# Kernel optimization log

Measured on AMD Instinct MI355X. Metric: run time of the kernel, lower is better.

The kernel has to match this reference:

```python
import jax, jax.numpy as jnp
import numpy as np

N_NODES = 50000
N_EDGES = 800000
HIDDEN = 64
NUM_FEATURES = 1
OUT_DIM = 2


def setup_inputs() -> dict:
    key = jax.random.key(0)
    k = jax.random.split(key, 6)
    x = jax.random.normal(k[0], (N_NODES, NUM_FEATURES), dtype=jnp.float32)
    edge_index = jax.random.randint(k[1], (2, N_EDGES), 0, N_NODES, dtype=jnp.int32)
    # GCNConv params (PyG default: glorot weight, zero bias; random here for testing)
    W1 = jax.random.normal(k[2], (NUM_FEATURES, HIDDEN), dtype=jnp.float32) * 0.5
    b1 = jax.random.normal(k[3], (HIDDEN,), dtype=jnp.float32) * 0.1
    W2 = jax.random.normal(k[4], (HIDDEN, OUT_DIM), dtype=jnp.float32) * 0.1
    b2 = jax.random.normal(k[5], (OUT_DIM,), dtype=jnp.float32) * 0.1
    return {"x": x, "edge_index": edge_index, "W1": W1, "b1": b1, "W2": W2, "b2": b2}


def _gcn_norm(edge_index, num_nodes):
    # PyG gcn_norm with add_self_loops=True, symmetric normalization
    row, col = edge_index[0], edge_index[1]
    loop = jnp.arange(num_nodes, dtype=row.dtype)
    row = jnp.concatenate([row, loop])
    col = jnp.concatenate([col, loop])
    ew = jnp.ones(row.shape[0], dtype=jnp.float32)
    deg = jax.ops.segment_sum(ew, col, num_segments=num_nodes)  # in-degree incl. self-loop
    dinv = jnp.where(deg > 0, jax.lax.rsqrt(deg), 0.0)
    norm = dinv[row] * dinv[col]  # [E+N]
    return row, col, norm


def _gcn_conv(x, row, col, norm, W, b, num_nodes):
    h = x @ W                                  # [N, out] transform first (out <= in here is fine)
    msg = h[row] * norm[:, None]               # gather + scale, [E+N, out]
    out = jax.ops.segment_sum(msg, col, num_segments=num_nodes)  # scatter-add at targets
    return out + b


def reference(x, edge_index, W1, b1, W2, b2):
    row, col, norm = _gcn_norm(edge_index, N_NODES)
    h = _gcn_conv(x, row, col, norm, W1, b1, N_NODES)
    h = jax.nn.relu(h)
    out = _gcn_conv(h, row, col, norm, W2, b2, N_NODES)
    return out
```

## Files before the change

### kernel.cpp

```cpp
#include <hip/hip_runtime.h>
#include <math.h>

#define N_NODES 50000
#define N_EDGES 800000
#define HIDDEN  64
#define NPART   500
#define PCHUNK  1600
#define NB      256
#define SL      196
#define CAPB    32
#define BCAP    3600


__global__ __launch_bounds__(256)
void k_part(const int* __restrict__ row, const int* __restrict__ col,
            unsigned* __restrict__ tails, unsigned* __restrict__ bks) {
    __shared__ unsigned stage[NB * CAPB];
    __shared__ unsigned cnt[NB], gpos[NB];
    const int t  = threadIdx.x;
    const int e0 = blockIdx.x * PCHUNK;
    cnt[t] = 0u;
    __syncthreads();
    const int4* c4 = (const int4*)(col + e0);
    const int4* r4 = (const int4*)(row + e0);
    for (int i = t; i < PCHUNK / 4; i += 256) {
        int4 cv = c4[i];
        int4 rv = r4[i];
#pragma unroll
        for (int k = 0; k < 4; ++k) {
            int c = (&cv.x)[k], r = (&rv.x)[k];
            int b = c / SL;
            unsigned off = atomicAdd(&cnt[b], 1u);
            if (off < CAPB)
                stage[(b << 5) + off] = ((unsigned)(c - b * SL) << 16) | (unsigned)r;
        }
    }
    __syncthreads();
    {
        unsigned cc = min(cnt[t], (unsigned)CAPB);
        cnt[t]  = cc;
        gpos[t] = atomicAdd(&tails[t], cc);
    }
    __syncthreads();
    for (int i = t; i < NB * CAPB; i += 256) {
        int b = i >> 5; unsigned o = (unsigned)(i & 31);
        if (o < cnt[b]) {
            unsigned dst = gpos[b] + o;
            if (dst < BCAP) bks[(size_t)b * BCAP + dst] = stage[i];
        }
    }
}

__global__ __launch_bounds__(256)
void k_dg(const unsigned* __restrict__ tails, const unsigned* __restrict__ bks,
          const float* __restrict__ x, float* __restrict__ dinv, float* __restrict__ g) {
    __shared__ unsigned acc[SL];
    const int t = threadIdx.x, b = blockIdx.x;
    if (t < SL) acc[t] = 0u;
    __syncthreads();
    unsigned tail = min(tails[b], (unsigned)BCAP);
    const unsigned* bk = bks + (size_t)b * BCAP;
    const uint4* bk4 = (const uint4*)bk;
    unsigned hv = tail & ~3u;
    for (unsigned i = t; (i << 2) < hv; i += 256) {
        uint4 v = bk4[i];
        atomicAdd(&acc[v.x >> 16], 1u);
        atomicAdd(&acc[v.y >> 16], 1u);
        atomicAdd(&acc[v.z >> 16], 1u);
        atomicAdd(&acc[v.w >> 16], 1u);
    }
    for (unsigned i = hv + t; i < tail; i += 256)
        atomicAdd(&acc[bk[i] >> 16], 1u);
    __syncthreads();
    if (t < SL) {
        int n = b * SL + t;
        if (n < N_NODES) {
            float di = rsqrtf((float)(acc[t] + 1u));
            dinv[n] = di;
            g[n] = di * x[n];
        }
    }
}

__global__ __launch_bounds__(256)
void k_a1(const unsigned* __restrict__ tails, const unsigned* __restrict__ bks,
          const float* __restrict__ g, const float* __restrict__ dinv,
          const float* __restrict__ W1, const float* __restrict__ b1,
          const float* __restrict__ W2, float2* __restrict__ z) {
    __shared__ float acc[SL];
    const int t = threadIdx.x, b = blockIdx.x;
    if (t < SL) acc[t] = 0.0f;
    __syncthreads();
    unsigned tail = min(tails[b], (unsigned)BCAP);
    const unsigned* bk = bks + (size_t)b * BCAP;
    const uint4* bk4 = (const uint4*)bk;
    unsigned hv = tail & ~3u;
    for (unsigned i = t; (i << 2) < hv; i += 256) {
        uint4 v = bk4[i];
        float g0 = g[v.x & 0xFFFFu];
        float g1 = g[v.y & 0xFFFFu];
        float g2 = g[v.z & 0xFFFFu];
        float g3 = g[v.w & 0xFFFFu];
        atomicAdd(&acc[v.x >> 16], g0);
        atomicAdd(&acc[v.y >> 16], g1);
        atomicAdd(&acc[v.z >> 16], g2);
        atomicAdd(&acc[v.w >> 16], g3);
    }
    for (unsigned i = hv + t; i < tail; i += 256) {
        unsigned v = bk[i];
        atomicAdd(&acc[v >> 16], g[v & 0xFFFFu]);
    }
    __syncthreads();
    if (t < SL) {
        int n = b * SL + t;
        if (n < N_NODES) {
            float di = dinv[n];
            float sv = di * (acc[t] + g[n]);
            float y0 = 0.0f, y1 = 0.0f;
#pragma unroll
            for (int k = 0; k < HIDDEN; ++k) {
                float h = fmaxf(sv * W1[k] + b1[k], 0.0f);
                y0 += h * W2[2 * k];
                y1 += h * W2[2 * k + 1];
            }
            z[n] = make_float2(di * y0, di * y1);
        }
    }
}

__global__ __launch_bounds__(256)
void k_a2(const unsigned* __restrict__ tails, const unsigned* __restrict__ bks,
          const float2* __restrict__ z, const float* __restrict__ dinv,
          const float* __restrict__ b2, float2* __restrict__ out) {
    __shared__ float ax[SL];
    __shared__ float ay[SL];
    const int t = threadIdx.x, b = blockIdx.x;
    if (t < SL) { ax[t] = 0.0f; ay[t] = 0.0f; }
    __syncthreads();
    unsigned tail = min(tails[b], (unsigned)BCAP);
    const unsigned* bk = bks + (size_t)b * BCAP;
    const uint4* bk4 = (const uint4*)bk;
    unsigned hv = tail & ~3u;
    for (unsigned i = t; (i << 2) < hv; i += 256) {
        uint4 v = bk4[i];
        float2 z0 = z[v.x & 0xFFFFu];
        float2 z1 = z[v.y & 0xFFFFu];
        float2 z2 = z[v.z & 0xFFFFu];
        float2 z3 = z[v.w & 0xFFFFu];
        atomicAdd(&ax[v.x >> 16], z0.x); atomicAdd(&ay[v.x >> 16], z0.y);
        atomicAdd(&ax[v.y >> 16], z1.x); atomicAdd(&ay[v.y >> 16], z1.y);
        atomicAdd(&ax[v.z >> 16], z2.x); atomicAdd(&ay[v.z >> 16], z2.y);
        atomicAdd(&ax[v.w >> 16], z3.x); atomicAdd(&ay[v.w >> 16], z3.y);
    }
    for (unsigned i = hv + t; i < tail; i += 256) {
        unsigned v = bk[i];
        float2 zz = z[v & 0xFFFFu];
        atomicAdd(&ax[v >> 16], zz.x);
        atomicAdd(&ay[v >> 16], zz.y);
    }
    __syncthreads();
    if (t < SL) {
        int n = b * SL + t;
        if (n < N_NODES) {
            float di = dinv[n];
            float2 zn = z[n];
            out[n] = make_float2(di * (ax[t] + zn.x) + b2[0],
                                 di * (ay[t] + zn.y) + b2[1]);
        }
    }
}


extern "C" void kernel_launch(void* const* d_in, const int* in_sizes, int n_in,
                              void* d_out, int out_size, void* d_ws, size_t ws_size,
                              hipStream_t stream) {
    const float* x  = (const float*)d_in[0];
    const int*   ei = (const int*)d_in[1];
    const float* W1 = (const float*)d_in[2];
    const float* b1 = (const float*)d_in[3];
    const float* W2 = (const float*)d_in[4];
    const float* b2 = (const float*)d_in[5];

    const int* row = ei;
    const int* col = ei + N_EDGES;

    char* p = (char*)d_ws;
    unsigned* tails = (unsigned*)p;  p += 1024 + 128;
    unsigned* bks   = (unsigned*)p;  p += (size_t)NB * BCAP * 4;
    float*    dinv  = (float*)p;     p += 200064;
    float*    g     = (float*)p;     p += 200064;
    float2*   z     = (float2*)p;

    hipMemsetAsync(tails, 0, NB * sizeof(unsigned), stream);
    k_part<<<NPART, 256, 0, stream>>>(row, col, tails, bks);
    k_dg  <<<NB,    256, 0, stream>>>(tails, bks, x, dinv, g);
    k_a1  <<<NB,    256, 0, stream>>>(tails, bks, g, dinv, W1, b1, W2, z);
    k_a2  <<<NB,    256, 0, stream>>>(tails, bks, z, dinv, b2, (float2*)d_out);
}
```

Before: 107.9 us.

## Fold degree counting into partition kernel and drop separate degree pass

Degree counting moves out of its own kernel into the partition kernel, which now does a global atomic increment per edge. The aggregation kernels recompute rsqrt(deg+1) and the x scaling per gathered source instead of reading precomputed dinv and g arrays. This removes one kernel launch and one extra pass over the bucketed edge lists. The cost is 800k global atomics spread over random addresses, plus two gathers and an rsqrt per edge in the first aggregation instead of one gather.

```diff
diff --git a/kernel.cpp b/kernel.cpp
--- a/kernel.cpp
+++ b/kernel.cpp
@@ -14,7 +14,8 @@
 
 __global__ __launch_bounds__(256)
 void k_part(const int* __restrict__ row, const int* __restrict__ col,
-            unsigned* __restrict__ tails, unsigned* __restrict__ bks) {
+            unsigned* __restrict__ tails, unsigned* __restrict__ bks,
+            unsigned* __restrict__ deg) {
     __shared__ unsigned stage[NB * CAPB];
     __shared__ unsigned cnt[NB], gpos[NB];
     const int t  = threadIdx.x;
@@ -29,6 +30,7 @@
 #pragma unroll
         for (int k = 0; k < 4; ++k) {
             int c = (&cv.x)[k], r = (&rv.x)[k];
+            atomicAdd(&deg[c], 1u);
             int b = c / SL;
             unsigned off = atomicAdd(&cnt[b], 1u);
             if (off < CAPB)
@@ -52,39 +54,8 @@
 }
 
 __global__ __launch_bounds__(256)
-void k_dg(const unsigned* __restrict__ tails, const unsigned* __restrict__ bks,
-          const float* __restrict__ x, float* __restrict__ dinv, float* __restrict__ g) {
-    __shared__ unsigned acc[SL];
-    const int t = threadIdx.x, b = blockIdx.x;
-    if (t < SL) acc[t] = 0u;
-    __syncthreads();
-    unsigned tail = min(tails[b], (unsigned)BCAP);
-    const unsigned* bk = bks + (size_t)b * BCAP;
-    const uint4* bk4 = (const uint4*)bk;
-    unsigned hv = tail & ~3u;
-    for (unsigned i = t; (i << 2) < hv; i += 256) {
-        uint4 v = bk4[i];
-        atomicAdd(&acc[v.x >> 16], 1u);
-        atomicAdd(&acc[v.y >> 16], 1u);
-        atomicAdd(&acc[v.z >> 16], 1u);
-        atomicAdd(&acc[v.w >> 16], 1u);
-    }
-    for (unsigned i = hv + t; i < tail; i += 256)
-        atomicAdd(&acc[bk[i] >> 16], 1u);
-    __syncthreads();
-    if (t < SL) {
-        int n = b * SL + t;
-        if (n < N_NODES) {
-            float di = rsqrtf((float)(acc[t] + 1u));
-            dinv[n] = di;
-            g[n] = di * x[n];
-        }
-    }
-}
-
-__global__ __launch_bounds__(256)
 void k_a1(const unsigned* __restrict__ tails, const unsigned* __restrict__ bks,
-          const float* __restrict__ g, const float* __restrict__ dinv,
+          const unsigned* __restrict__ deg, const float* __restrict__ x,
           const float* __restrict__ W1, const float* __restrict__ b1,
           const float* __restrict__ W2, float2* __restrict__ z) {
     __shared__ float acc[SL];
@@ -97,25 +68,31 @@
     unsigned hv = tail & ~3u;
     for (unsigned i = t; (i << 2) < hv; i += 256) {
         uint4 v = bk4[i];
-        float g0 = g[v.x & 0xFFFFu];
-        float g1 = g[v.y & 0xFFFFu];
-        float g2 = g[v.z & 0xFFFFu];
-        float g3 = g[v.w & 0xFFFFu];
-        atomicAdd(&acc[v.x >> 16], g0);
-        atomicAdd(&acc[v.y >> 16], g1);
-        atomicAdd(&acc[v.z >> 16], g2);
-        atomicAdd(&acc[v.w >> 16], g3);
+        unsigned r0 = v.x & 0xFFFFu, r1 = v.y & 0xFFFFu,
+                 r2 = v.z & 0xFFFFu, r3 = v.w & 0xFFFFu;
+        unsigned d0 = deg[r0], d1 = deg[r1], d2 = deg[r2], d3 = deg[r3];
+        float x0 = x[r0], x1 = x[r1], x2 = x[r2], x3 = x[r3];
+        float m0 = rsqrtf((float)(d0 + 1u)) * x0;
+        float m1 = rsqrtf((float)(d1 + 1u)) * x1;
+        float m2 = rsqrtf((float)(d2 + 1u)) * x2;
+        float m3 = rsqrtf((float)(d3 + 1u)) * x3;
+        atomicAdd(&acc[v.x >> 16], m0);
+        atomicAdd(&acc[v.y >> 16], m1);
+        atomicAdd(&acc[v.z >> 16], m2);
+        atomicAdd(&acc[v.w >> 16], m3);
     }
     for (unsigned i = hv + t; i < tail; i += 256) {
         unsigned v = bk[i];
-        atomicAdd(&acc[v >> 16], g[v & 0xFFFFu]);
+        unsigned r = v & 0xFFFFu;
+        float m = rsqrtf((float)(deg[r] + 1u)) * x[r];
+        atomicAdd(&acc[v >> 16], m);
     }
     __syncthreads();
     if (t < SL) {
         int n = b * SL + t;
         if (n < N_NODES) {
-            float di = dinv[n];
-            float sv = di * (acc[t] + g[n]);
+            float di = rsqrtf((float)(deg[n] + 1u));
+            float sv = di * (acc[t] + di * x[n]);
             float y0 = 0.0f, y1 = 0.0f;
 #pragma unroll
             for (int k = 0; k < HIDDEN; ++k) {
@@ -130,7 +107,7 @@
 
 __global__ __launch_bounds__(256)
 void k_a2(const unsigned* __restrict__ tails, const unsigned* __restrict__ bks,
-          const float2* __restrict__ z, const float* __restrict__ dinv,
+          const unsigned* __restrict__ deg, const float2* __restrict__ z,
           const float* __restrict__ b2, float2* __restrict__ out) {
     __shared__ float ax[SL];
     __shared__ float ay[SL];
@@ -162,7 +139,7 @@
     if (t < SL) {
         int n = b * SL + t;
         if (n < N_NODES) {
-            float di = dinv[n];
+            float di = rsqrtf((float)(deg[n] + 1u));
             float2 zn = z[n];
             out[n] = make_float2(di * (ax[t] + zn.x) + b2[0],
                                  di * (ay[t] + zn.y) + b2[1]);
@@ -185,15 +162,13 @@
     const int* col = ei + N_EDGES;
 
     char* p = (char*)d_ws;
-    unsigned* tails = (unsigned*)p;  p += 1024 + 128;
+    unsigned* deg   = (unsigned*)p;  p += 50176 * 4;
+    unsigned* tails = (unsigned*)p;  p += 1024;
     unsigned* bks   = (unsigned*)p;  p += (size_t)NB * BCAP * 4;
-    float*    dinv  = (float*)p;     p += 200064;
-    float*    g     = (float*)p;     p += 200064;
     float2*   z     = (float2*)p;
 
-    hipMemsetAsync(tails, 0, NB * sizeof(unsigned), stream);
-    k_part<<<NPART, 256, 0, stream>>>(row, col, tails, bks);
-    k_dg  <<<NB,    256, 0, stream>>>(tails, bks, x, dinv, g);
-    k_a1  <<<NB,    256, 0, stream>>>(tails, bks, g, dinv, W1, b1, W2, z);
-    k_a2  <<<NB,    256, 0, stream>>>(tails, bks, z, dinv, b2, (float2*)d_out);
+    hipMemsetAsync(deg, 0, 50176 * 4 + 1024, stream);
+    k_part<<<NPART, 256, 0, stream>>>(row, col, tails, bks, deg);
+    k_a1  <<<NB,    256, 0, stream>>>(tails, bks, deg, x, W1, b1, W2, z);
+    k_a2  <<<NB,    256, 0, stream>>>(tails, bks, deg, z, b2, (float2*)d_out);
 }
```

New measurement: 135.8 us. +25.9%, slower.
